# Performance work log

Measured on AMD Instinct MI355X. Metric: run time of the kernel, lower is better.

Reference implementation:

```python
import jax, jax.numpy as jnp
import numpy as np

N_PROBLEMS = 20000
N_SKILLS = 1000
EMB_SIZE = 128
TIME_LOG = 5.0
B, L = 64, 1024


def setup_inputs() -> dict:
    key = jax.random.key(0)
    ks = jax.random.split(key, 10)
    skills = jax.random.randint(ks[0], (B, L), 0, N_SKILLS)
    problems = jax.random.randint(ks[1], (B, L), 0, N_PROBLEMS)
    labels = jax.random.randint(ks[2], (B, L), 0, 2)
    times = jnp.sort(jax.random.randint(ks[3], (B, L), 0, 1_000_000), axis=-1)
    inp = jnp.stack([skills, problems, labels, times], axis=1)  # [B,4,L]
    std = 0.01
    return {
        "input": inp,
        "problem_base": std * jax.random.normal(ks[4], (N_PROBLEMS, 1), jnp.float32),
        "skill_base": std * jax.random.normal(ks[5], (N_SKILLS, 1), jnp.float32),
        "alpha_inter": std * jax.random.normal(ks[6], (N_SKILLS * 2, EMB_SIZE), jnp.float32),
        "alpha_skill": std * jax.random.normal(ks[7], (N_SKILLS, EMB_SIZE), jnp.float32),
        "beta_inter": std * jax.random.normal(ks[8], (N_SKILLS * 2, EMB_SIZE), jnp.float32),
        "beta_skill": std * jax.random.normal(ks[9], (N_SKILLS, EMB_SIZE), jnp.float32),
    }


def reference(input, problem_base, skill_base, alpha_inter, alpha_skill, beta_inter, beta_skill):
    skills = input[:, 0]    # [B,L]
    problems = input[:, 1]
    labels = input[:, 2]
    times = input[:, 3]

    mask_labels = labels * (labels < 2).astype(labels.dtype)
    inters = skills + mask_labels * N_SKILLS  # [B,L] in [0, 2*N_SKILLS)

    # pairwise Hawkes excitation / decay scores: [B,L,L]
    alphas = jnp.einsum('bie,bje->bij', alpha_inter[inters], alpha_skill[skills])
    betas = jnp.einsum('bie,bje->bij', beta_inter[inters], beta_skill[skills])
    betas = jnp.clip(betas + 1.0, 0.0, 10.0)

    dt = jnp.abs(times[:, :, None] - times[:, None, :]).astype(jnp.float32)
    log_dt = jnp.log(dt + 1e-10) / np.log(TIME_LOG)

    cross_effects = alphas * jnp.exp(-betas * log_dt)

    seq_len = skills.shape[1]
    # keep strictly-upper-triangular entries (source i before target j)
    keep = jnp.triu(jnp.ones((seq_len, seq_len), dtype=bool), k=1)
    sum_t = jnp.where(keep[None], cross_effects, 0.0).sum(axis=-2)  # [B,L]

    problem_bias = problem_base[problems][..., 0]
    skill_bias = skill_base[skills][..., 0]
    return jax.nn.sigmoid(problem_bias + skill_bias + sum_t)
```

## Files before the change

### kernel.cpp

```cpp
#include <hip/hip_runtime.h>
#include <hip/hip_bf16.h>

#define NB   64
#define SL   1024
#define EMB  128
#define NSK  1000
#define TI   64
#define NS   2

#define AI_OFF 0
#define BI_OFF 256000
#define AS_OFF 512000
#define BS_OFF 640000
#define TB_ELEMS 768000
#define ACC_BYTE_OFF (TB_ELEMS * 2)

using short8  = __attribute__((ext_vector_type(8))) short;
using floatx4 = __attribute__((ext_vector_type(4))) float;

#define INV_LOG2_5 0.43067655807339306f

__device__ inline unsigned cvt2(float x, float y) {
    float2 f; f.x = x; f.y = y;
    __hip_bfloat162 h = __float22bfloat162_rn(f);
    unsigned u; __builtin_memcpy(&u, &h, sizeof(u));
    return u;
}

extern "C" __global__ __launch_bounds__(256)
void cvt_tables(const float* __restrict__ ai, const float* __restrict__ bi,
                const float* __restrict__ as, const float* __restrict__ bs,
                unsigned short* __restrict__ dst)
{
    const int t = blockIdx.x * 256 + threadIdx.x;
    const long e = (long)t * 8;
    const float* src;
    if      (e < 256000) src = ai + e;
    else if (e < 512000) src = bi + (e - 256000);
    else if (e < 640000) src = as + (e - 512000);
    else                 src = bs + (e - 640000);
    float4 f0 = *(const float4*)src;
    float4 f1 = *(const float4*)(src + 4);
    uint4 pk;
    pk.x = cvt2(f0.x, f0.y); pk.y = cvt2(f0.z, f0.w);
    pk.z = cvt2(f1.x, f1.y); pk.w = cvt2(f1.z, f1.w);
    *(uint4*)(dst + e) = pk;
}

__device__ float fixup_pair(const float* __restrict__ air,
                            const float* __restrict__ bir,
                            const float* __restrict__ asr,
                            const float* __restrict__ bsr) {
    float da = 0.f, db = 0.f;
#pragma unroll 8
    for (int k = 0; k < EMB; k += 4) {
        float4 a  = *(const float4*)(air + k);
        float4 s  = *(const float4*)(asr + k);
        float4 bq = *(const float4*)(bir + k);
        float4 tt = *(const float4*)(bsr + k);
        da += a.x * s.x + a.y * s.y + a.z * s.z + a.w * s.w;
        db += bq.x * tt.x + bq.y * tt.y + bq.z * tt.z + bq.w * tt.w;
    }
    float beta = fminf(fmaxf(db + 1.f, 0.f), 10.f);
    return da * __expf(beta * 14.30676558073393f);
}

struct Stage { uint4 a0, a1, a2, a3; };

__device__ __forceinline__ Stage stage_load(const int* __restrict__ binp,
                                            const unsigned short* __restrict__ tb,
                                            int ib, int row, int m, int sq)
{
    const int irow  = ib + row;
    const int ski   = binp[irow];
    const int li    = binp[2 * SL + irow];
    const long intr = ski + (long)li * NSK;
    const unsigned short* src = tb + (m ? BI_OFF : AI_OFF) + intr * EMB + sq * 32;
    Stage s;
    s.a0 = *(const uint4*)(src);
    s.a1 = *(const uint4*)(src + 8);
    s.a2 = *(const uint4*)(src + 16);
    s.a3 = *(const uint4*)(src + 24);
    return s;
}

__device__ __forceinline__ void stage_write(char* buf, int wbase, const Stage& s) {
    *(uint4*)(buf + wbase)              = s.a0;
    *(uint4*)(buf + wbase + 128)        = s.a1;
    *(uint4*)(buf + (wbase ^ 16))       = s.a2;
    *(uint4*)(buf + (wbase ^ 16) + 128) = s.a3;
}

__device__ __forceinline__ float phase_compute(const char* __restrict__ buf,
                                               const int* __restrict__ binp,
                                               const short8 bfa[4], const short8 bfb[4],
                                               const int roff[4],
                                               int ib, int tj, int quad)
{
    float psum = 0.f;
#pragma unroll
    for (int isub = 0; isub < 2; ++isub) {
        floatx4 aa = {0.f, 0.f, 0.f, 0.f};
        floatx4 bb = {1.f, 1.f, 1.f, 1.f};
#pragma unroll
        for (int ks = 0; ks < 4; ++ks) {
            short8 av = *(const short8*)(buf + isub * 4096 + roff[ks]);
            short8 bv = *(const short8*)(buf + 8192 + isub * 4096 + roff[ks]);
            aa = __builtin_amdgcn_mfma_f32_16x16x32_bf16(av, bfa[ks], aa, 0, 0, 0);
            bb = __builtin_amdgcn_mfma_f32_16x16x32_bf16(bv, bfb[ks], bb, 0, 0, 0);
        }
        const int ibase = ib + isub * 16 + quad * 4;
        const int4 t4 = *(const int4*)(binp + 3 * SL + ibase);
#pragma unroll
        for (int rr = 0; rr < 4; ++rr) {
            const int ti = (rr == 0) ? t4.x : (rr == 1) ? t4.y : (rr == 2) ? t4.z : t4.w;
            const int dt = tj - ti;
            float lc  = __log2f((float)dt);
            float nb  = fminf(fmaxf(bb[rr], 0.f), 10.f) * (-INV_LOG2_5);
            float arg = (dt > 0) ? nb * lc : -__builtin_inff();
            psum += aa[rr] * __builtin_amdgcn_exp2f(arg);
        }
    }
    return psum;
}

extern "C" __global__ __launch_bounds__(256, 4)
void hawkes_main(const int*   __restrict__ inp,
                 const unsigned short* __restrict__ tb,
                 float*       __restrict__ acc)
{
    __shared__ uint4 lds4[2048];
    char* ldsc = (char*)lds4;

    const int bid  = blockIdx.x;
    const int b    = bid & (NB - 1);
    const int r    = bid >> 6;
    const int jt   = 15 - (r >> 1);
    const int s    = r & 1;
    const int tid  = threadIdx.x;
    const int w    = tid >> 6;
    const int l    = tid & 63;
    const int quad = l >> 4;
    const int col  = l & 15;

    const int* __restrict__ binp = inp + b * 4 * SL;

    const int jlane = jt * TI + w * 16 + col;
    const int sk_j  = binp[jlane];
    const int tj    = binp[3 * SL + jlane];

    short8 bfa[4], bfb[4];
    {
        const unsigned short* asr16 = tb + AS_OFF + (long)sk_j * EMB + quad * 8;
        const unsigned short* bsr16 = tb + BS_OFF + (long)sk_j * EMB + quad * 8;
#pragma unroll
        for (int ks = 0; ks < 4; ++ks) {
            bfa[ks] = *(const short8*)(asr16 + ks * 32);
            bfb[ks] = *(const short8*)(bsr16 + ks * 32);
        }
    }

    int roff[4];
    {
        const int qh = quad >> 1, ql = quad & 1, c7 = col & 7;
#pragma unroll
        for (int ks = 0; ks < 4; ++ks)
            roff[ks] = col * 256 + ql * 128 + (((2 * ks + qh) ^ c7) << 4);
    }

    const int ri    = tid >> 2;
    const int m     = ri >> 5;
    const int row   = ri & 31;
    const int sq    = tid & 3;
    const int wbase = m * 8192 + row * 256 + ((((2 * sq) ^ (row & 7))) << 4);

    float sum = 0.f;

    if (s <= jt) {
        const int ntiles = ((jt - s) >> 1) + 1;
        int ib = s * TI;

        Stage rA = stage_load(binp, tb, ib, row, m, sq);
        stage_write(ldsc, wbase, rA);
        Stage rB = stage_load(binp, tb, ib + 32, row, m, sq);

        for (int t = 0; t < ntiles; ++t) {
            const int ibn   = ib + NS * TI;
            const bool more = (t + 1 < ntiles);

            __syncthreads();
            stage_write(ldsc + 16384, wbase, rB);
            if (more) rA = stage_load(binp, tb, ibn, row, m, sq);
            sum += phase_compute(ldsc, binp, bfa, bfb, roff, ib, tj, quad);

            __syncthreads();
            if (more) {
                stage_write(ldsc, wbase, rA);
                rB = stage_load(binp, tb, ibn + 32, row, m, sq);
            }
            sum += phase_compute(ldsc + 16384, binp, bfa, bfb, roff, ib + 32, tj, quad);

            ib = ibn;
        }
    }

    sum += __shfl_xor(sum, 16, 64);
    sum += __shfl_xor(sum, 32, 64);

    if (quad == 0) {
        acc[(((long)s * NB + b) << 10) + jlane] = sum;
    }
}

extern "C" __global__ __launch_bounds__(256)
void hawkes_finalize(const int* __restrict__ inp, const float* __restrict__ pbase,
                     const float* __restrict__ sbase,
                     const float* __restrict__ ai, const float* __restrict__ as,
                     const float* __restrict__ bi, const float* __restrict__ bs,
                     const float* __restrict__ acc, float* __restrict__ out)
{
    const int t = blockIdx.x * 256 + threadIdx.x;
    const int b = t >> 10, j = t & (SL - 1);
    const int* binp = inp + b * 4 * SL;
    const int tj   = binp[3 * SL + j];
    const int sk_j = binp[j];

    float corr = 0.f;
    for (int i = j - 1; i >= 0 && binp[3 * SL + i] == tj; --i) {
        const int ski = binp[i], li = binp[2 * SL + i];
        const long intr = ski + (long)li * NSK;
        corr += fixup_pair(ai + intr * EMB, bi + intr * EMB,
                           as + (long)sk_j * EMB, bs + (long)sk_j * EMB);
    }

    float sum = acc[t] + acc[NB * SL + t] + corr;
    const float x = pbase[binp[SL + j]] + sbase[sk_j] + sum;
    out[t] = 1.f / (1.f + __expf(-x));
}

extern "C" void kernel_launch(void* const* d_in, const int* in_sizes, int n_in,
                              void* d_out, int out_size, void* d_ws, size_t ws_size,
                              hipStream_t stream) {
    const int*   inp = (const int*)d_in[0];
    const float* pb  = (const float*)d_in[1];
    const float* sb  = (const float*)d_in[2];
    const float* ai  = (const float*)d_in[3];
    const float* as  = (const float*)d_in[4];
    const float* bi  = (const float*)d_in[5];
    const float* bs  = (const float*)d_in[6];

    unsigned short* tb  = (unsigned short*)d_ws;
    float*          acc = (float*)((char*)d_ws + ACC_BYTE_OFF);

    cvt_tables<<<dim3(96000 / 256), dim3(256), 0, stream>>>(ai, bi, as, bs, tb);
    hawkes_main<<<dim3(NB * 16 * NS), dim3(256), 0, stream>>>(inp, tb, acc);
    hawkes_finalize<<<dim3(NB * SL / 256), dim3(256), 0, stream>>>(
        inp, pb, sb, ai, as, bi, bs, acc, (float*)d_out);
}
```

Measured before the change: 116.2 us.

## Fuse finalize into main Hawkes kernel and drop split-K accumulation

Removes the two-way split over source tiles. Each block now walks all source tiles for its target tile and applies the equal-timestamp fixup, biases and sigmoid itself, so the separate finalize kernel and the partial-sum workspace round trip go away. This saves one launch and the global accumulator traffic. In exchange the grid is halved and the heaviest blocks process twice as many tiles sequentially, which lengthens the critical path and worsens load imbalance across the triangular workload. Staging is also reorganised into byte-offset half-tile loads, and all LDS fragment reads are issued before the MFMAs.

```diff
diff --git a/kernel.cpp b/kernel.cpp
--- a/kernel.cpp
+++ b/kernel.cpp
@@ -6,14 +6,13 @@
 #define EMB  128
 #define NSK  1000
 #define TI   64
-#define NS   2
-
-#define AI_OFF 0
-#define BI_OFF 256000
-#define AS_OFF 512000
-#define BS_OFF 640000
+
 #define TB_ELEMS 768000
-#define ACC_BYTE_OFF (TB_ELEMS * 2)
+
+#define AI_B 0
+#define BI_B 512000
+#define AS_B 1024000
+#define BS_B 1280000
 
 using short8  = __attribute__((ext_vector_type(8))) short;
 using floatx4 = __attribute__((ext_vector_type(4))) float;
@@ -65,78 +64,45 @@
     return da * __expf(beta * 14.30676558073393f);
 }
 
-struct Stage { uint4 a0, a1, a2, a3; };
-
-__device__ __forceinline__ Stage stage_load(const int* __restrict__ binp,
-                                            const unsigned short* __restrict__ tb,
-                                            int ib, int row, int m, int sq)
-{
-    const int irow  = ib + row;
-    const int ski   = binp[irow];
-    const int li    = binp[2 * SL + irow];
-    const long intr = ski + (long)li * NSK;
-    const unsigned short* src = tb + (m ? BI_OFF : AI_OFF) + intr * EMB + sq * 32;
-    Stage s;
-    s.a0 = *(const uint4*)(src);
-    s.a1 = *(const uint4*)(src + 8);
-    s.a2 = *(const uint4*)(src + 16);
-    s.a3 = *(const uint4*)(src + 24);
+struct StageH { uint4 q0, q1, q2, q3; };
+
+__device__ __forceinline__ StageH stageh_load(const int* __restrict__ binp,
+                                              const char* __restrict__ tbc,
+                                              int half, int row, long matb, int sq)
+{
+    const int arow = half * 32 + row;
+    const long intr = binp[arow] + (long)binp[2 * SL + arow] * NSK;
+    const char* p = tbc + matb + intr * 256 + sq * 64;
+    StageH s;
+    s.q0 = *(const uint4*)(p);      s.q1 = *(const uint4*)(p + 16);
+    s.q2 = *(const uint4*)(p + 32); s.q3 = *(const uint4*)(p + 48);
     return s;
 }
 
-__device__ __forceinline__ void stage_write(char* buf, int wbase, const Stage& s) {
-    *(uint4*)(buf + wbase)              = s.a0;
-    *(uint4*)(buf + wbase + 128)        = s.a1;
-    *(uint4*)(buf + (wbase ^ 16))       = s.a2;
-    *(uint4*)(buf + (wbase ^ 16) + 128) = s.a3;
-}
-
-__device__ __forceinline__ float phase_compute(const char* __restrict__ buf,
-                                               const int* __restrict__ binp,
-                                               const short8 bfa[4], const short8 bfb[4],
-                                               const int roff[4],
-                                               int ib, int tj, int quad)
-{
-    float psum = 0.f;
-#pragma unroll
-    for (int isub = 0; isub < 2; ++isub) {
-        floatx4 aa = {0.f, 0.f, 0.f, 0.f};
-        floatx4 bb = {1.f, 1.f, 1.f, 1.f};
-#pragma unroll
-        for (int ks = 0; ks < 4; ++ks) {
-            short8 av = *(const short8*)(buf + isub * 4096 + roff[ks]);
-            short8 bv = *(const short8*)(buf + 8192 + isub * 4096 + roff[ks]);
-            aa = __builtin_amdgcn_mfma_f32_16x16x32_bf16(av, bfa[ks], aa, 0, 0, 0);
-            bb = __builtin_amdgcn_mfma_f32_16x16x32_bf16(bv, bfb[ks], bb, 0, 0, 0);
-        }
-        const int ibase = ib + isub * 16 + quad * 4;
-        const int4 t4 = *(const int4*)(binp + 3 * SL + ibase);
-#pragma unroll
-        for (int rr = 0; rr < 4; ++rr) {
-            const int ti = (rr == 0) ? t4.x : (rr == 1) ? t4.y : (rr == 2) ? t4.z : t4.w;
-            const int dt = tj - ti;
-            float lc  = __log2f((float)dt);
-            float nb  = fminf(fmaxf(bb[rr], 0.f), 10.f) * (-INV_LOG2_5);
-            float arg = (dt > 0) ? nb * lc : -__builtin_inff();
-            psum += aa[rr] * __builtin_amdgcn_exp2f(arg);
-        }
-    }
-    return psum;
+__device__ __forceinline__ void stageh_write(char* buf, int row, long matoff,
+                                             int wslot, const StageH& s)
+{
+    char* p  = buf + matoff + row * 256 + wslot;
+    char* px = buf + matoff + row * 256 + (wslot ^ 16);
+    *(uint4*)(p)        = s.q0;  *(uint4*)(p + 128)  = s.q1;
+    *(uint4*)(px)       = s.q2;  *(uint4*)(px + 128) = s.q3;
 }
 
 extern "C" __global__ __launch_bounds__(256, 4)
-void hawkes_main(const int*   __restrict__ inp,
-                 const unsigned short* __restrict__ tb,
-                 float*       __restrict__ acc)
-{
-    __shared__ uint4 lds4[2048];
-    char* ldsc = (char*)lds4;
+void hawkes_fused(const int*   __restrict__ inp,
+                  const unsigned short* __restrict__ tb,
+                  const float* __restrict__ pbase,
+                  const float* __restrict__ sbase,
+                  const float* __restrict__ ai, const float* __restrict__ as,
+                  const float* __restrict__ bi, const float* __restrict__ bs,
+                  float*       __restrict__ out)
+{
+    __shared__ uint4 ldsq[2048];
+    char* ldsc = (char*)ldsq;
 
     const int bid  = blockIdx.x;
     const int b    = bid & (NB - 1);
-    const int r    = bid >> 6;
-    const int jt   = 15 - (r >> 1);
-    const int s    = r & 1;
+    const int jt   = 15 - (bid >> 6);
     const int tid  = threadIdx.x;
     const int w    = tid >> 6;
     const int l    = tid & 63;
@@ -144,6 +110,7 @@
     const int col  = l & 15;
 
     const int* __restrict__ binp = inp + b * 4 * SL;
+    const char* __restrict__ tbc = (const char*)tb;
 
     const int jlane = jt * TI + w * 16 + col;
     const int sk_j  = binp[jlane];
@@ -151,14 +118,20 @@
 
     short8 bfa[4], bfb[4];
     {
-        const unsigned short* asr16 = tb + AS_OFF + (long)sk_j * EMB + quad * 8;
-        const unsigned short* bsr16 = tb + BS_OFF + (long)sk_j * EMB + quad * 8;
+        const char* asr = tbc + AS_B + (long)sk_j * 256 + quad * 16;
+        const char* bsr = tbc + BS_B + (long)sk_j * 256 + quad * 16;
 #pragma unroll
         for (int ks = 0; ks < 4; ++ks) {
-            bfa[ks] = *(const short8*)(asr16 + ks * 32);
-            bfb[ks] = *(const short8*)(bsr16 + ks * 32);
+            bfa[ks] = *(const short8*)(asr + ks * 64);
+            bfb[ks] = *(const short8*)(bsr + ks * 64);
         }
     }
+
+    const int  srow  = tid >> 3;
+    const long matb  = ((tid >> 2) & 1) ? (long)BI_B : (long)AI_B;
+    const long matoff = ((tid >> 2) & 1) ? 8192 : 0;
+    const int  sq    = tid & 3;
+    const int  wslot = (((2 * sq) ^ (srow & 7)) << 4);
 
     int roff[4];
     {
@@ -168,39 +141,59 @@
             roff[ks] = col * 256 + ql * 128 + (((2 * ks + qh) ^ c7) << 4);
     }
 
-    const int ri    = tid >> 2;
-    const int m     = ri >> 5;
-    const int row   = ri & 31;
-    const int sq    = tid & 3;
-    const int wbase = m * 8192 + row * 256 + ((((2 * sq) ^ (row & 7))) << 4);
-
+    const int nh = 2 * (jt + 1);
     float sum = 0.f;
 
-    if (s <= jt) {
-        const int ntiles = ((jt - s) >> 1) + 1;
-        int ib = s * TI;
-
-        Stage rA = stage_load(binp, tb, ib, row, m, sq);
-        stage_write(ldsc, wbase, rA);
-        Stage rB = stage_load(binp, tb, ib + 32, row, m, sq);
-
-        for (int t = 0; t < ntiles; ++t) {
-            const int ibn   = ib + NS * TI;
-            const bool more = (t + 1 < ntiles);
-
+    StageH sEven = stageh_load(binp, tbc, 0, srow, matb, sq);
+    stageh_write(ldsc, srow, matoff, wslot, sEven);
+    StageH sOdd;
+    if (nh > 1) sOdd = stageh_load(binp, tbc, 1, srow, matb, sq);
+
+#pragma unroll 1
+    for (int t = 0; t <= jt; ++t) {
+        const int h2 = 2 * t + 2;
+
+#pragma unroll
+        for (int ph = 0; ph < 2; ++ph) {
             __syncthreads();
-            stage_write(ldsc + 16384, wbase, rB);
-            if (more) rA = stage_load(binp, tb, ibn, row, m, sq);
-            sum += phase_compute(ldsc, binp, bfa, bfb, roff, ib, tj, quad);
-
-            __syncthreads();
-            if (more) {
-                stage_write(ldsc, wbase, rA);
-                rB = stage_load(binp, tb, ibn + 32, row, m, sq);
+            if (ph == 0) {
+                stageh_write(ldsc + 16384, srow, matoff, wslot, sOdd);
+                if (h2 < nh) sEven = stageh_load(binp, tbc, h2, srow, matb, sq);
+            } else {
+                if (h2 < nh)     stageh_write(ldsc, srow, matoff, wslot, sEven);
+                if (h2 + 1 < nh) sOdd = stageh_load(binp, tbc, h2 + 1, srow, matb, sq);
             }
-            sum += phase_compute(ldsc + 16384, binp, bfa, bfb, roff, ib + 32, tj, quad);
-
-            ib = ibn;
+
+            const char* buf     = ldsc + (ph ? 16384 : 0);
+            const int   rowbase = t * 64 + ph * 32;
+
+#pragma unroll
+            for (int isub = 0; isub < 2; ++isub) {
+                short8 av[4], bv[4];
+#pragma unroll
+                for (int ks = 0; ks < 4; ++ks) {
+                    av[ks] = *(const short8*)(buf + isub * 4096 + roff[ks]);
+                    bv[ks] = *(const short8*)(buf + 8192 + isub * 4096 + roff[ks]);
+                }
+                const int4 t4 = *(const int4*)(binp + 3 * SL + rowbase + isub * 16 + quad * 4);
+
+                floatx4 aa = {0.f, 0.f, 0.f, 0.f};
+                floatx4 bb = {1.f, 1.f, 1.f, 1.f};
+#pragma unroll
+                for (int ks = 0; ks < 4; ++ks) {
+                    aa = __builtin_amdgcn_mfma_f32_16x16x32_bf16(av[ks], bfa[ks], aa, 0, 0, 0);
+                    bb = __builtin_amdgcn_mfma_f32_16x16x32_bf16(bv[ks], bfb[ks], bb, 0, 0, 0);
+                }
+#pragma unroll
+                for (int rr = 0; rr < 4; ++rr) {
+                    const int ti = (rr == 0) ? t4.x : (rr == 1) ? t4.y : (rr == 2) ? t4.z : t4.w;
+                    const int dt = tj - ti;
+                    float lc  = __log2f((float)dt);
+                    float nb  = fminf(fmaxf(bb[rr], 0.f), 10.f) * (-INV_LOG2_5);
+                    float arg = (dt > 0) ? nb * lc : -__builtin_inff();
+                    sum += aa[rr] * __builtin_amdgcn_exp2f(arg);
+                }
+            }
         }
     }
 
@@ -208,34 +201,16 @@
     sum += __shfl_xor(sum, 32, 64);
 
     if (quad == 0) {
-        acc[(((long)s * NB + b) << 10) + jlane] = sum;
-    }
-}
-
-extern "C" __global__ __launch_bounds__(256)
-void hawkes_finalize(const int* __restrict__ inp, const float* __restrict__ pbase,
-                     const float* __restrict__ sbase,
-                     const float* __restrict__ ai, const float* __restrict__ as,
-                     const float* __restrict__ bi, const float* __restrict__ bs,
-                     const float* __restrict__ acc, float* __restrict__ out)
-{
-    const int t = blockIdx.x * 256 + threadIdx.x;
-    const int b = t >> 10, j = t & (SL - 1);
-    const int* binp = inp + b * 4 * SL;
-    const int tj   = binp[3 * SL + j];
-    const int sk_j = binp[j];
-
-    float corr = 0.f;
-    for (int i = j - 1; i >= 0 && binp[3 * SL + i] == tj; --i) {
-        const int ski = binp[i], li = binp[2 * SL + i];
-        const long intr = ski + (long)li * NSK;
-        corr += fixup_pair(ai + intr * EMB, bi + intr * EMB,
-                           as + (long)sk_j * EMB, bs + (long)sk_j * EMB);
-    }
-
-    float sum = acc[t] + acc[NB * SL + t] + corr;
-    const float x = pbase[binp[SL + j]] + sbase[sk_j] + sum;
-    out[t] = 1.f / (1.f + __expf(-x));
+        float corr = 0.f;
+        for (int i = jlane - 1; i >= 0 && binp[3 * SL + i] == tj; --i) {
+            const int ski = binp[i], li = binp[2 * SL + i];
+            const long intr = ski + (long)li * NSK;
+            corr += fixup_pair(ai + intr * EMB, bi + intr * EMB,
+                               as + (long)sk_j * EMB, bs + (long)sk_j * EMB);
+        }
+        const float x = pbase[binp[SL + jlane]] + sbase[sk_j] + sum + corr;
+        out[b * SL + jlane] = 1.f / (1.f + __expf(-x));
+    }
 }
 
 extern "C" void kernel_launch(void* const* d_in, const int* in_sizes, int n_in,
@@ -249,11 +224,9 @@
     const float* bi  = (const float*)d_in[5];
     const float* bs  = (const float*)d_in[6];
 
-    unsigned short* tb  = (unsigned short*)d_ws;
-    float*          acc = (float*)((char*)d_ws + ACC_BYTE_OFF);
+    unsigned short* tb = (unsigned short*)d_ws;
 
     cvt_tables<<<dim3(96000 / 256), dim3(256), 0, stream>>>(ai, bi, as, bs, tb);
-    hawkes_main<<<dim3(NB * 16 * NS), dim3(256), 0, stream>>>(inp, tb, acc);
-    hawkes_finalize<<<dim3(NB * SL / 256), dim3(256), 0, stream>>>(
-        inp, pb, sb, ai, as, bi, bs, acc, (float*)d_out);
-}
+    hawkes_fused<<<dim3(16 * NB), dim3(256), 0, stream>>>(
+        inp, tb, pb, sb, ai, as, bi, bs, (float*)d_out);
+}
```

Result: no change. 115.0 us (-1.0%).
